# Performance work log

Hardware: AMD Instinct MI355X
Metric: run time of the kernel (lower is better)

## Reference

```python
import jax, jax.numpy as jnp
import numpy as np
from jax import lax

NPOINT = 1024
RADIUS = 0.2
NSAMPLE = 32
BN_EPS = 1e-3  # tf_util batch_norm variance_epsilon


def setup_inputs() -> dict:
    key = jax.random.key(0)
    ks = jax.random.split(key, 16)
    B, N, Cp = 8, 4096, 64
    mlp = [64, 64, 128]
    cin = 3 + Cp  # use_xyz=True concatenates local coords
    dk, dout = 128, 128
    inp = {}
    inp["xyz"] = jax.random.uniform(ks[0], (B, N, 3), jnp.float32)
    inp["points"] = jax.random.normal(ks[1], (B, N, Cp), jnp.float32)
    dims = [cin] + mlp
    for i in range(3):
        inp[f"W{i}"] = jax.random.normal(ks[2 + i], (dims[i], dims[i + 1]), jnp.float32) / np.sqrt(dims[i]).astype(np.float32)
        inp[f"b{i}"] = jnp.zeros((dims[i + 1],), jnp.float32)
        inp[f"g{i}"] = jnp.ones((dims[i + 1],), jnp.float32)
        inp[f"be{i}"] = jnp.zeros((dims[i + 1],), jnp.float32)
    inp["Wq"] = jax.random.normal(ks[10], (3, dk), jnp.float32) * 0.1
    inp["Wk"] = jax.random.normal(ks[11], (mlp[-1], dk), jnp.float32) * 0.1
    inp["Wv"] = jax.random.normal(ks[12], (mlp[-1], dout), jnp.float32) * 0.1
    return inp


def farthest_point_sample(xyz, npoint):
    # xyz: [B, N, 3] -> idx [B, npoint] (sequential FPS, seeded at point 0)
    B, N, _ = xyz.shape

    def body(carry, _):
        dist, farthest = carry  # dist [B,N], farthest [B]
        centroid = jnp.take_along_axis(xyz, farthest[:, None, None], axis=1)  # [B,1,3]
        d = jnp.sum((xyz - centroid) ** 2, axis=-1)  # [B,N]
        dist = jnp.minimum(dist, d)
        nxt = jnp.argmax(dist, axis=-1).astype(jnp.int32)
        return (dist, nxt), farthest

    init = (jnp.full((B, N), 1e10, xyz.dtype), jnp.zeros((B,), jnp.int32))
    _, idxs = lax.scan(body, init, None, length=npoint)
    return jnp.transpose(idxs)  # [B, npoint]


def query_ball_point(radius, nsample, xyz, new_xyz):
    # first `nsample` points (in index order) within radius; pad with first hit
    N = xyz.shape[1]
    d2 = jnp.sum((new_xyz[:, :, None, :] - xyz[:, None, :, :]) ** 2, axis=-1)  # [B,S,N]
    inball = d2 < radius * radius
    ar = jnp.arange(N, dtype=jnp.int32)
    order_key = jnp.where(inball, ar, ar + N)
    idx = jnp.argsort(order_key, axis=-1)[..., :nsample].astype(jnp.int32)  # [B,S,nsample]
    valid = jnp.take_along_axis(inball, idx, axis=-1)
    idx = jnp.where(valid, idx, idx[..., :1])
    return idx


def group_point(feat, idx):
    # feat [B,N,C], idx [B,S,K] -> [B,S,K,C]
    return jax.vmap(lambda f, i: f[i])(feat, idx)


def _conv_bn_relu(x, W, b, g, be):
    y = jnp.einsum('bskc,cd->bskd', x, W) + b  # 1x1 conv == pointwise linear
    mean = jnp.mean(y, axis=(0, 1, 2))
    var = jnp.var(y, axis=(0, 1, 2))
    y = (y - mean) * g * lax.rsqrt(var + BN_EPS) + be
    return jax.nn.relu(y)


def _forward(xyz, points, Ws, bs, gs, bes, Wq, Wk, Wv):
    fps_idx = farthest_point_sample(xyz, NPOINT)                 # [B,S]
    new_xyz = jnp.take_along_axis(xyz, fps_idx[..., None], 1)    # [B,S,3]
    idx = query_ball_point(RADIUS, NSAMPLE, xyz, new_xyz)        # [B,S,K]
    grouped_xyz = group_point(xyz, idx) - new_xyz[:, :, None, :]  # local coords
    grouped_pts = group_point(points, idx)
    new_points = jnp.concatenate([grouped_xyz, grouped_pts], axis=-1)  # [B,S,K,3+C]
    for W, b, g, be in zip(Ws, bs, gs, bes):
        new_points = _conv_bn_relu(new_points, W, b, g, be)
    # attention pooling over the K neighbors, query from group center coords
    dk = Wq.shape[1]
    q = new_xyz @ Wq                                         # [B,S,dk]
    k = jnp.einsum('bskc,cd->bskd', new_points, Wk)          # [B,S,K,dk]
    v = jnp.einsum('bskc,co->bsko', new_points, Wv)          # [B,S,K,out]
    scores = jax.nn.softmax(jnp.einsum('bsd,bskd->bsk', q, k) / jnp.sqrt(jnp.float32(dk)), axis=-1)
    pooled = jnp.einsum('bsk,bsko->bso', scores, v)          # [B,S,out]
    return new_xyz, pooled, idx


def reference(xyz, points, W0, b0, g0, be0, W1, b1, g1, be1, W2, b2, g2, be2, Wq, Wk, Wv):
    return _forward(xyz, points, (W0, W1, W2), (b0, b1, b2), (g0, g1, g2), (be0, be1, be2), Wq, Wk, Wv)
```

## Files before the change

kernel.cpp:

```cpp
#include <hip/hip_runtime.h>
#include <hip/hip_bf16.h>

#define DI __device__ __forceinline__

typedef __attribute__((ext_vector_type(8))) short bf16x8;
typedef __attribute__((ext_vector_type(4))) float f32x4;

DI float fmulr(float a, float b){ return __fmul_rn(a,b); }
DI float faddr(float a, float b){ return __fadd_rn(a,b); }
DI float fsubr(float a, float b){ return __fsub_rn(a,b); }
DI float dist2e(float x,float y,float z,float cx,float cy,float cz){
  float dx=fsubr(x,cx), dy=fsubr(y,cy), dz=fsubr(z,cz);
  return faddr(faddr(fmulr(dx,dx),fmulr(dy,dy)),fmulr(dz,dz));
}
DI unsigned short f2bf(float f){ __hip_bfloat16 h=__float2bfloat16(f); return *reinterpret_cast<unsigned short*>(&h); }
DI unsigned long long umax64(unsigned long long a, unsigned long long b){ return a>b?a:b; }

template<int C> DI float dmax_step(float x){
  int y=__builtin_amdgcn_update_dpp(0, __float_as_int(x), C, 0xF, 0xF, true);
  return fmaxf(x, __int_as_float(y));
}

__global__ __launch_bounds__(512) void fps_kernel(const float* __restrict__ xyz, float* __restrict__ out0){
  extern __shared__ char smem[];
  float4* sp4=(float4*)smem;
  float* spf=(float*)smem;
  unsigned long long* keys=(unsigned long long*)(smem+65536);
  int b=blockIdx.x, tid=threadIdx.x;
  const float* xb = xyz + (size_t)b*12288;
  for(int e=tid;e<12288;e+=512){ int p=e/3, c=e-3*p; spf[4*p+c]=xb[e]; }
  __syncthreads();
  float px[8],py[8],pz[8],dist[8];
  int p0=tid*8;
  #pragma unroll
  for(int j=0;j<8;j++){ float4 r=sp4[p0+j]; px[j]=r.x; py[j]=r.y; pz[j]=r.z; dist[j]=1e10f; }
  int cur=0;
  float4 cc0=sp4[0];
  float cx=cc0.x, cy=cc0.y, cz=cc0.z;
  int w=tid>>6, lane=tid&63;
  int c0s=0,c1s=0;
  float* ob = out0 + (size_t)b*1024*3;
  #pragma unroll 1
  for(int t=0;t<1024;t++){
    bool mine=((t&511)==tid);
    int hi=t>>9;
    c0s=(mine&&hi==0)?cur:c0s;
    c1s=(mine&&hi==1)?cur:c1s;
    float nd[8];
    #pragma unroll
    for(int j=0;j<8;j++){
      float d=dist2e(px[j],py[j],pz[j],cx,cy,cz);
      float m=fminf(dist[j],d); dist[j]=m; nd[j]=m;
    }
    float a0=fmaxf(nd[0],nd[1]), a1=fmaxf(nd[2],nd[3]), a2=fmaxf(nd[4],nd[5]), a3=fmaxf(nd[6],nd[7]);
    float bv=fmaxf(fmaxf(a0,a1),fmaxf(a2,a3));
    unsigned msk=0u;
    #pragma unroll
    for(int j=0;j<8;j++) msk |= (nd[j]==bv)?(1u<<j):0u;
    int bj=__ffs(msk)-1;
    int bi=p0+bj;
    float x=bv;
    x=dmax_step<0x111>(x); x=dmax_step<0x112>(x); x=dmax_step<0x114>(x); x=dmax_step<0x118>(x);
    x=dmax_step<0x142>(x); x=dmax_step<0x143>(x);
    float wv=__int_as_float(__builtin_amdgcn_readlane(__float_as_int(x),63));
    unsigned long long em=__ballot(bv==wv);
    int L=(int)(__ffsll(em)-1);
    int wbi=__builtin_amdgcn_readlane(bi,L);
    int par=t&1;
    if(lane==0){
      keys[par*8+w] = ((unsigned long long)__float_as_uint(wv)<<32)
                    | (unsigned long long)(0xFFFFFFFFu-(unsigned)wbi);
    }
    __syncthreads();
    const ulonglong2* sl2=(const ulonglong2*)(keys+par*8);
    ulonglong2 k0=sl2[0], k1=sl2[1], k2=sl2[2], k3=sl2[3];
    unsigned long long m0=umax64(k0.x,k0.y), m1=umax64(k1.x,k1.y);
    unsigned long long m2=umax64(k2.x,k2.y), m3=umax64(k3.x,k3.y);
    unsigned long long k =umax64(umax64(m0,m1),umax64(m2,m3));
    cur=(int)(0xFFFFFFFFu-(unsigned)(k&0xFFFFFFFFull));
    float4 cc=sp4[cur]; cx=cc.x; cy=cc.y; cz=cc.z;
  }
  { int t0=tid;     float4 c=sp4[c0s]; ob[t0*3]=c.x; ob[t0*3+1]=c.y; ob[t0*3+2]=c.z; }
  { int t1=tid+512; float4 c=sp4[c1s]; ob[t1*3]=c.x; ob[t1*3+1]=c.y; ob[t1*3+2]=c.z; }
}

__global__ __launch_bounds__(256) void ballq_kernel(const float* __restrict__ xyz, const float* __restrict__ out0,
        int* __restrict__ idxw, float* __restrict__ out2){
  __shared__ float sp[12288];
  int tid=threadIdx.x;
  int g = blockIdx.x*4 + (tid>>6);
  int lane = tid&63;
  int b = blockIdx.x>>8;
  const float* xb = xyz + (size_t)b*4096*3;
  const float4* src=(const float4*)xb; float4* dst=(float4*)sp;
  #pragma unroll
  for(int i=0;i<12;i++) dst[i*256+tid]=src[i*256+tid];
  __syncthreads();
  float cx=out0[(size_t)g*3], cy=out0[(size_t)g*3+1], cz=out0[(size_t)g*3+2];
  const float R2 = (float)(0.2*0.2);
  int cnt=0, firstp=0; bool haveFirst=false;
  for(int c=0;c<64;c++){
    int p=c*64+lane;
    float x=sp[3*p], y=sp[3*p+1], z=sp[3*p+2];
    float d2=dist2e(x,y,z,cx,cy,cz);
    bool inb = d2 < R2;
    unsigned long long mask=__ballot(inb);
    if(!haveFirst && mask){ firstp = c*64 + (__ffsll((unsigned long long)mask)-1); haveFirst=true; }
    int pos = cnt + (int)__popcll(mask & ((1ull<<lane)-1ull));
    if(inb && pos<32){ idxw[(size_t)g*32+pos]=p; out2[(size_t)g*32+pos]=(float)p; }
    cnt += (int)__popcll(mask);
    if(cnt>=32) break;
  }
  if(cnt<32){
    for(int j=cnt+lane; j<32; j+=64){ idxw[(size_t)g*32+j]=firstp; out2[(size_t)g*32+j]=(float)firstp; }
  }
}

__global__ void m_kernel(const float* __restrict__ Wq, const float* __restrict__ Wk, float* __restrict__ M){
  int c = threadIdx.x;
  float m0=0.f,m1=0.f,m2=0.f;
  for(int d=0; d<128; d++){
    float wk = Wk[c*128+d];
    m0 += Wq[d]*wk; m1 += Wq[128+d]*wk; m2 += Wq[256+d]*wk;
  }
  M[c]=m0; M[128+c]=m1; M[256+c]=m2;
}

__global__ __launch_bounds__(256) void l0_mfma(const float* __restrict__ xyz, const float* __restrict__ pts,
    const float* __restrict__ out0, const int* __restrict__ idxw,
    const float* __restrict__ W0, const float* __restrict__ b0,
    __hip_bfloat16* __restrict__ y0, float* __restrict__ P){
  __shared__ unsigned short xg[64*72];
  __shared__ unsigned short wt[64*72];
  __shared__ unsigned short yt[64*72];
  __shared__ float xyzl[64][4];
  __shared__ float w0c[3][64];
  __shared__ float ps[4][64];
  __shared__ float qs[4][64];
  int tid=threadIdx.x; int base=blockIdx.x*64;
  int w=tid>>6, lane=tid&63;
  for(int i=0;i<16;i++){
    int r=w*16+i; int R=base+r;
    int g=R>>5; int b=g>>10; int p=idxw[R];
    xg[r*72+lane] = f2bf(pts[((size_t)b*4096+(size_t)p)*64+lane]);
    if(lane<3) xyzl[r][lane] = fsubr(xyz[((size_t)b*4096+(size_t)p)*3+lane], out0[(size_t)g*3+lane]);
  }
  for(int e=tid; e<4096; e+=256){
    int k=e>>6, n=e&63;
    wt[n*72+k]=f2bf(W0[(3+k)*64+n]);
  }
  if(tid<192){ int r=tid>>6, n=tid&63; w0c[r][n]=W0[r*64+n]; }
  __syncthreads();
  int m=lane&15, kg=lane>>4;
  f32x4 acc[4];
  #pragma unroll
  for(int t=0;t<4;t++){
    int col=t*16+m;
    float bb=b0[col], wx=w0c[0][col], wy=w0c[1][col], wz=w0c[2][col];
    #pragma unroll
    for(int rg=0;rg<4;rg++){
      int row=w*16+kg*4+rg;
      acc[t][rg]=bb + xyzl[row][0]*wx + xyzl[row][1]*wy + xyzl[row][2]*wz;
    }
  }
  #pragma unroll
  for(int ks=0; ks<2; ks++){
    int k0=ks*32+kg*8;
    bf16x8 af = *(bf16x8*)&xg[(w*16+m)*72 + k0];
    #pragma unroll
    for(int t=0;t<4;t++){
      bf16x8 bfr = *(bf16x8*)&wt[(t*16+m)*72 + k0];
      acc[t]=__builtin_amdgcn_mfma_f32_16x16x32_bf16(af,bfr,acc[t],0,0,0);
    }
  }
  #pragma unroll
  for(int t=0;t<4;t++){
    float s=0.f,q=0.f;
    #pragma unroll
    for(int rg=0;rg<4;rg++){
      float v=acc[t][rg];
      s+=v; q+=v*v;
      yt[(w*16+kg*4+rg)*72 + t*16+m]=f2bf(v);
    }
    s+=__shfl_xor(s,16); q+=__shfl_xor(q,16);
    s+=__shfl_xor(s,32); q+=__shfl_xor(q,32);
    if(kg==0){ ps[w][t*16+m]=s; qs[w][t*16+m]=q; }
  }
  __syncthreads();
  if(tid<64){
    float s=ps[0][tid]+ps[1][tid]+ps[2][tid]+ps[3][tid];
    float q=qs[0][tid]+qs[1][tid]+qs[2][tid]+qs[3][tid];
    P[(size_t)tid*4096+blockIdx.x]=s;
    P[(size_t)(128+tid)*4096+blockIdx.x]=q;
  }
  for(int e=tid; e<512; e+=256){
    int r=e>>3, c0=(e&7)*8;
    *reinterpret_cast<uint4*>(y0 + ((size_t)base+r)*64 + c0) = *reinterpret_cast<uint4*>(&yt[r*72+c0]);
  }
}

template<int CIN,int COUT>
__global__ __launch_bounds__(256) void lmid_mfma(const __hip_bfloat16* __restrict__ xin,
    const float* __restrict__ ssIn, const float* __restrict__ W, const float* __restrict__ bias,
    __hip_bfloat16* __restrict__ yout, float* __restrict__ P){
  constexpr int XS = CIN+8;
  constexpr int YS = COUT+8;
  constexpr int NT = COUT/16;
  __shared__ unsigned short xt[64*XS];
  __shared__ unsigned short wt[COUT*XS];
  __shared__ unsigned short yt[64*YS];
  __shared__ float ps[4][COUT];
  __shared__ float qs[4][COUT];
  int tid=threadIdx.x; size_t base=(size_t)blockIdx.x*64;
  int w=tid>>6, lane=tid&63;
  for(int e=tid; e<64*CIN/8; e+=256){
    int r=e/(CIN/8), c0=(e%(CIN/8))*8;
    uint4 raw = *reinterpret_cast<const uint4*>(xin + (base+(size_t)r)*CIN + c0);
    unsigned u[4]={raw.x,raw.y,raw.z,raw.w};
    unsigned short* dst=&xt[r*XS+c0];
    #pragma unroll
    for(int k2=0;k2<4;k2++){
      int c=c0+2*k2;
      float lo=__uint_as_float(u[k2]<<16);
      float hi=__uint_as_float(u[k2]&0xFFFF0000u);
      float a=lo*ssIn[c]+ssIn[128+c]; a=a>0.f?a:0.f;
      float bq=hi*ssIn[c+1]+ssIn[128+c+1]; bq=bq>0.f?bq:0.f;
      dst[2*k2]=f2bf(a); dst[2*k2+1]=f2bf(bq);
    }
  }
  for(int e=tid; e<CIN*COUT; e+=256){
    int k=e/COUT, n=e-k*COUT;
    wt[n*XS+k]=f2bf(W[e]);
  }
  __syncthreads();
  f32x4 acc[NT];
  #pragma unroll
  for(int t=0;t<NT;t++) acc[t]=(f32x4){0.f,0.f,0.f,0.f};
  int m=lane&15, kg=lane>>4;
  #pragma unroll
  for(int ks=0; ks<CIN/32; ks++){
    int k0=ks*32+kg*8;
    bf16x8 af = *(bf16x8*)&xt[(w*16+m)*XS + k0];
    #pragma unroll
    for(int t=0;t<NT;t++){
      bf16x8 bfr = *(bf16x8*)&wt[(t*16+m)*XS + k0];
      acc[t]=__builtin_amdgcn_mfma_f32_16x16x32_bf16(af,bfr,acc[t],0,0,0);
    }
  }
  #pragma unroll
  for(int t=0;t<NT;t++){
    float bv=bias[t*16+m];
    float s=0.f,q=0.f;
    #pragma unroll
    for(int rg=0;rg<4;rg++){
      float v=acc[t][rg]+bv;
      s+=v; q+=v*v;
      yt[(w*16+kg*4+rg)*YS + t*16+m]=f2bf(v);
    }
    s+=__shfl_xor(s,16); q+=__shfl_xor(q,16);
    s+=__shfl_xor(s,32); q+=__shfl_xor(q,32);
    if(kg==0){ ps[w][t*16+m]=s; qs[w][t*16+m]=q; }
  }
  __syncthreads();
  if(tid<COUT){
    float s=ps[0][tid]+ps[1][tid]+ps[2][tid]+ps[3][tid];
    float q=qs[0][tid]+qs[1][tid]+qs[2][tid]+qs[3][tid];
    P[(size_t)tid*4096+blockIdx.x]=s;
    P[(size_t)(128+tid)*4096+blockIdx.x]=q;
  }
  for(int e=tid; e<64*COUT/8; e+=256){
    int r=e/(COUT/8), c0=(e%(COUT/8))*8;
    *reinterpret_cast<uint4*>(yout + (base+(size_t)r)*COUT + c0) = *reinterpret_cast<uint4*>(&yt[r*YS+c0]);
  }
}

__global__ void fin_kernel(const float* __restrict__ P, const float* __restrict__ gg, const float* __restrict__ be,
                           float* __restrict__ ss){
  int ch=blockIdx.x; int lane=threadIdx.x;
  float s=0.f,q=0.f;
  for(int blk=lane; blk<4096; blk+=64){ s+=P[(size_t)ch*4096+blk]; q+=P[(size_t)(128+ch)*4096+blk]; }
  #pragma unroll
  for(int m=32;m>=1;m>>=1){ s+=__shfl_xor(s,m); q+=__shfl_xor(q,m); }
  if(lane==0){
    const float invNT = 1.0f/262144.0f;
    float mean=s*invNT; float var=q*invNT - mean*mean;
    float scale=gg[ch]/sqrtf(var+1e-3f);
    ss[ch]=scale; ss[128+ch]=be[ch]-mean*scale;
  }
}

__global__ __launch_bounds__(256) void sh_kernel(const __hip_bfloat16* __restrict__ y2,
    const float* __restrict__ ss2, const float* __restrict__ M, const float* __restrict__ out0,
    float* __restrict__ hbar){
  __shared__ float h[2][32*130];
  __shared__ float uLds[2][128];
  __shared__ float sLds[2][32];
  __shared__ float partLds[2][4][32];
  int tid=threadIdx.x; int grp=tid>>7, t=tid&127;
  size_t g=(size_t)blockIdx.x*2+grp;
  #pragma unroll
  for(int i=0;i<4;i++){
    int e=i*128+t;
    int row=e>>4, c0=(e&15)*8;
    uint4 raw=*reinterpret_cast<const uint4*>(y2+(g*32+(size_t)row)*128+c0);
    unsigned u[4]={raw.x,raw.y,raw.z,raw.w};
    #pragma unroll
    for(int k=0;k<4;k++){
      int c=c0+2*k;
      float lo=__uint_as_float(u[k]<<16), hi=__uint_as_float(u[k]&0xFFFF0000u);
      float a=lo*ss2[c]+ss2[128+c]; float bq=hi*ss2[c+1]+ss2[128+c+1];
      h[grp][row*130+c]  = a>0.f?a:0.f;
      h[grp][row*130+c+1]= bq>0.f?bq:0.f;
    }
  }
  float cx=out0[g*3], cy=out0[g*3+1], cz=out0[g*3+2];
  uLds[grp][t]=cx*M[t]+cy*M[128+t]+cz*M[256+t];
  __syncthreads();
  {
    int row=t&31, q=t>>5;
    float sc=0.f;
    const float* hr=&h[grp][row*130];
    const float* ur=&uLds[grp][0];
    #pragma unroll
    for(int c=0;c<32;c++) sc += hr[q*32+c]*ur[q*32+c];
    partLds[grp][q][row]=sc;
  }
  __syncthreads();
  if(t<32){
    float s=(partLds[grp][0][t]+partLds[grp][1][t])+(partLds[grp][2][t]+partLds[grp][3][t]);
    s*=0.08838834764831845f;
    float mx=s;
    #pragma unroll
    for(int m=16;m>=1;m>>=1) mx=fmaxf(mx,__shfl_xor(mx,m));
    float p=expf(s-mx);
    float sum=p;
    #pragma unroll
    for(int m=16;m>=1;m>>=1) sum+=__shfl_xor(sum,m);
    sLds[grp][t]=p/sum;
  }
  __syncthreads();
  float hb=0.f;
  for(int k=0;k<32;k++) hb+=sLds[grp][k]*h[grp][k*130+t];
  hbar[g*128+t]=hb;
}

__global__ __launch_bounds__(256) void pool_kernel(const float* __restrict__ hbar, const float* __restrict__ Wv,
    float* __restrict__ out1){
  __shared__ float xl[32*129];
  int tid=threadIdx.x; size_t g0=(size_t)blockIdx.x*32;
  for(int e=tid;e<32*128;e+=256){ int r=e>>7,ch=e&127; xl[r*129+ch]=hbar[(g0+(size_t)r)*128+ch]; }
  __syncthreads();
  int r=tid&31;
  int cgu=__builtin_amdgcn_readfirstlane(tid>>5);
  float acc[16];
  #pragma unroll
  for(int j=0;j<16;j++) acc[j]=0.f;
  for(int c=0;c<128;c++){
    float xv=xl[r*129+c];
    #pragma unroll
    for(int j=0;j<16;j++) acc[j]+=xv*Wv[c*128+cgu*16+j];
  }
  #pragma unroll
  for(int j=0;j<16;j++) out1[(g0+(size_t)r)*128+cgu*16+j]=acc[j];
}

extern "C" void kernel_launch(void* const* d_in, const int* in_sizes, int n_in,
                              void* d_out, int out_size, void* d_ws, size_t ws_size,
                              hipStream_t stream){
  (void)in_sizes; (void)n_in; (void)out_size; (void)ws_size;
  const float* xyz=(const float*)d_in[0];
  const float* pts=(const float*)d_in[1];
  const float* W0=(const float*)d_in[2];  const float* b0=(const float*)d_in[3];
  const float* g0=(const float*)d_in[4];  const float* be0=(const float*)d_in[5];
  const float* W1=(const float*)d_in[6];  const float* b1=(const float*)d_in[7];
  const float* g1=(const float*)d_in[8];  const float* be1=(const float*)d_in[9];
  const float* W2=(const float*)d_in[10]; const float* b2=(const float*)d_in[11];
  const float* g2=(const float*)d_in[12]; const float* be2=(const float*)d_in[13];
  const float* Wq=(const float*)d_in[14]; const float* Wk=(const float*)d_in[15];
  const float* Wv=(const float*)d_in[16];
  float* out0=(float*)d_out;
  float* out1=out0 + (size_t)8*1024*3;
  float* out2=out1 + (size_t)8192*128;

  char* ws=(char*)d_ws; size_t off=0;
  int* idxw=(int*)(ws+off);                    off += (size_t)8192*32*4;
  __hip_bfloat16* fa=(__hip_bfloat16*)(ws+off); off += (size_t)262144*64*2;
  __hip_bfloat16* fb=(__hip_bfloat16*)(ws+off); off += (size_t)262144*64*2;
  __hip_bfloat16* fc=(__hip_bfloat16*)(ws+off); off += (size_t)262144*128*2;
  float* P =(float*)(ws+off);                  off += (size_t)256*4096*4;
  float* ss0=(float*)(ws+off);                 off += 256*4;
  float* ss1=(float*)(ws+off);                 off += 256*4;
  float* ss2=(float*)(ws+off);                 off += 256*4;
  float* M =(float*)(ws+off);                  off += 3*128*4 + 128;
  float* hb=(float*)(ws+off);                  off += (size_t)8192*128*4;

  hipLaunchKernelGGL(fps_kernel,   dim3(8),    dim3(512), 65536+128, stream, xyz, out0);
  hipLaunchKernelGGL(ballq_kernel, dim3(2048), dim3(256),  0, stream, xyz, out0, idxw, out2);
  hipLaunchKernelGGL(m_kernel,     dim3(1),    dim3(128),  0, stream, Wq, Wk, M);
  hipLaunchKernelGGL(l0_mfma,      dim3(4096), dim3(256),  0, stream, xyz, pts, out0, idxw, W0, b0, fa, P);
  hipLaunchKernelGGL(fin_kernel,   dim3(64),   dim3(64),   0, stream, P, g0, be0, ss0);
  hipLaunchKernelGGL((lmid_mfma<64,64>),  dim3(4096), dim3(256), 0, stream, fa, ss0, W1, b1, fb, P);
  hipLaunchKernelGGL(fin_kernel,   dim3(64),   dim3(64),   0, stream, P, g1, be1, ss1);
  hipLaunchKernelGGL((lmid_mfma<64,128>), dim3(4096), dim3(256), 0, stream, fb, ss1, W2, b2, fc, P);
  hipLaunchKernelGGL(fin_kernel,   dim3(128),  dim3(64),   0, stream, P, g2, be2, ss2);
  hipLaunchKernelGGL(sh_kernel,    dim3(4096), dim3(256),  0, stream, fc, ss2, M, out0, hb);
  hipLaunchKernelGGL(pool_kernel,  dim3(256),  dim3(256),  0, stream, hb, Wv, out1);
}
```

Baseline: 891.0 us.

## Halve FPS block to four waves and broadcast winner coords; cache BN scales in LDS

```diff
diff --git a/kernel.cpp b/kernel.cpp
--- a/kernel.cpp
+++ b/kernel.cpp
@@ -14,49 +14,53 @@
   return faddr(faddr(fmulr(dx,dx),fmulr(dy,dy)),fmulr(dz,dz));
 }
 DI unsigned short f2bf(float f){ __hip_bfloat16 h=__float2bfloat16(f); return *reinterpret_cast<unsigned short*>(&h); }
-DI unsigned long long umax64(unsigned long long a, unsigned long long b){ return a>b?a:b; }
 
 template<int C> DI float dmax_step(float x){
   int y=__builtin_amdgcn_update_dpp(0, __float_as_int(x), C, 0xF, 0xF, true);
   return fmaxf(x, __int_as_float(y));
 }
 
-__global__ __launch_bounds__(512) void fps_kernel(const float* __restrict__ xyz, float* __restrict__ out0){
+__global__ __launch_bounds__(256) void fps_kernel(const float* __restrict__ xyz, float* __restrict__ out0){
   extern __shared__ char smem[];
   float4* sp4=(float4*)smem;
   float* spf=(float*)smem;
   unsigned long long* keys=(unsigned long long*)(smem+65536);
+  float4* wco=(float4*)(smem+65536+64);
   int b=blockIdx.x, tid=threadIdx.x;
   const float* xb = xyz + (size_t)b*12288;
-  for(int e=tid;e<12288;e+=512){ int p=e/3, c=e-3*p; spf[4*p+c]=xb[e]; }
-  __syncthreads();
-  float px[8],py[8],pz[8],dist[8];
-  int p0=tid*8;
-  #pragma unroll
-  for(int j=0;j<8;j++){ float4 r=sp4[p0+j]; px[j]=r.x; py[j]=r.y; pz[j]=r.z; dist[j]=1e10f; }
+  for(int e=tid;e<12288;e+=256){ int p=e/3, c=e-3*p; spf[4*p+c]=xb[e]; }
+  __syncthreads();
+  float px[16],py[16],pz[16],dist[16];
+  int p0 = tid*16;
+  #pragma unroll
+  for(int j=0;j<16;j++){ float4 r=sp4[p0+j]; px[j]=r.x; py[j]=r.y; pz[j]=r.z; dist[j]=1e10f; }
   int cur=0;
   float4 cc0=sp4[0];
   float cx=cc0.x, cy=cc0.y, cz=cc0.z;
   int w=tid>>6, lane=tid&63;
-  int c0s=0,c1s=0;
+  int c0s=0,c1s=0,c2s=0,c3s=0;
   float* ob = out0 + (size_t)b*1024*3;
   #pragma unroll 1
   for(int t=0;t<1024;t++){
-    bool mine=((t&511)==tid);
-    int hi=t>>9;
-    c0s=(mine&&hi==0)?cur:c0s;
-    c1s=(mine&&hi==1)?cur:c1s;
-    float nd[8];
-    #pragma unroll
-    for(int j=0;j<8;j++){
+    bool mine = ((t&255)==tid);
+    int hi = t>>8;
+    c0s = (mine && hi==0) ? cur : c0s;
+    c1s = (mine && hi==1) ? cur : c1s;
+    c2s = (mine && hi==2) ? cur : c2s;
+    c3s = (mine && hi==3) ? cur : c3s;
+    float nd[16];
+    #pragma unroll
+    for(int j=0;j<16;j++){
       float d=dist2e(px[j],py[j],pz[j],cx,cy,cz);
       float m=fminf(dist[j],d); dist[j]=m; nd[j]=m;
     }
     float a0=fmaxf(nd[0],nd[1]), a1=fmaxf(nd[2],nd[3]), a2=fmaxf(nd[4],nd[5]), a3=fmaxf(nd[6],nd[7]);
-    float bv=fmaxf(fmaxf(a0,a1),fmaxf(a2,a3));
+    float a4=fmaxf(nd[8],nd[9]), a5=fmaxf(nd[10],nd[11]), a6=fmaxf(nd[12],nd[13]), a7=fmaxf(nd[14],nd[15]);
+    float b0=fmaxf(a0,a1), b1=fmaxf(a2,a3), b2=fmaxf(a4,a5), b3=fmaxf(a6,a7);
+    float bv=fmaxf(fmaxf(b0,b1),fmaxf(b2,b3));
     unsigned msk=0u;
     #pragma unroll
-    for(int j=0;j<8;j++) msk |= (nd[j]==bv)?(1u<<j):0u;
+    for(int j=0;j<16;j++) msk |= (nd[j]==bv) ? (1u<<j) : 0u;
     int bj=__ffs(msk)-1;
     int bi=p0+bj;
     float x=bv;
@@ -65,23 +69,29 @@
     float wv=__int_as_float(__builtin_amdgcn_readlane(__float_as_int(x),63));
     unsigned long long em=__ballot(bv==wv);
     int L=(int)(__ffsll(em)-1);
-    int wbi=__builtin_amdgcn_readlane(bi,L);
     int par=t&1;
-    if(lane==0){
-      keys[par*8+w] = ((unsigned long long)__float_as_uint(wv)<<32)
-                    | (unsigned long long)(0xFFFFFFFFu-(unsigned)wbi);
+    if(lane==L){
+      keys[par*4+w] = ((unsigned long long)__float_as_uint(wv)<<32)
+                    | (unsigned long long)(0xFFFFFFFFu-(unsigned)bi);
+      wco[par*4+w]  = make_float4(px[bj],py[bj],pz[bj],0.f);
     }
     __syncthreads();
-    const ulonglong2* sl2=(const ulonglong2*)(keys+par*8);
-    ulonglong2 k0=sl2[0], k1=sl2[1], k2=sl2[2], k3=sl2[3];
-    unsigned long long m0=umax64(k0.x,k0.y), m1=umax64(k1.x,k1.y);
-    unsigned long long m2=umax64(k2.x,k2.y), m3=umax64(k3.x,k3.y);
-    unsigned long long k =umax64(umax64(m0,m1),umax64(m2,m3));
+    ulonglong2 ka=*(const ulonglong2*)(keys+par*4);
+    ulonglong2 kb=*(const ulonglong2*)(keys+par*4+2);
+    float4 q0=wco[par*4+0], q1=wco[par*4+1], q2=wco[par*4+2], q3=wco[par*4+3];
+    bool s01 = ka.x>=ka.y; unsigned long long k01 = s01?ka.x:ka.y;
+    bool s23 = kb.x>=kb.y; unsigned long long k23 = s23?kb.x:kb.y;
+    float c01x=s01?q0.x:q1.x, c01y=s01?q0.y:q1.y, c01z=s01?q0.z:q1.z;
+    float c23x=s23?q2.x:q3.x, c23y=s23?q2.y:q3.y, c23z=s23?q2.z:q3.z;
+    bool sf = k01>=k23;
+    unsigned long long k = sf?k01:k23;
+    cx = sf?c01x:c23x; cy = sf?c01y:c23y; cz = sf?c01z:c23z;
     cur=(int)(0xFFFFFFFFu-(unsigned)(k&0xFFFFFFFFull));
-    float4 cc=sp4[cur]; cx=cc.x; cy=cc.y; cz=cc.z;
   }
   { int t0=tid;     float4 c=sp4[c0s]; ob[t0*3]=c.x; ob[t0*3+1]=c.y; ob[t0*3+2]=c.z; }
-  { int t1=tid+512; float4 c=sp4[c1s]; ob[t1*3]=c.x; ob[t1*3+1]=c.y; ob[t1*3+2]=c.z; }
+  { int t1=tid+256; float4 c=sp4[c1s]; ob[t1*3]=c.x; ob[t1*3+1]=c.y; ob[t1*3+2]=c.z; }
+  { int t2=tid+512; float4 c=sp4[c2s]; ob[t2*3]=c.x; ob[t2*3+1]=c.y; ob[t2*3+2]=c.z; }
+  { int t3=tid+768; float4 c=sp4[c3s]; ob[t3*3]=c.x; ob[t3*3+1]=c.y; ob[t3*3+2]=c.z; }
 }
 
 __global__ __launch_bounds__(256) void ballq_kernel(const float* __restrict__ xyz, const float* __restrict__ out0,
@@ -211,8 +221,11 @@
   __shared__ unsigned short yt[64*YS];
   __shared__ float ps[4][COUT];
   __shared__ float qs[4][COUT];
+  __shared__ float ssl[256];
   int tid=threadIdx.x; size_t base=(size_t)blockIdx.x*64;
   int w=tid>>6, lane=tid&63;
+  ssl[tid]=ssIn[tid];
+  __syncthreads();
   for(int e=tid; e<64*CIN/8; e+=256){
     int r=e/(CIN/8), c0=(e%(CIN/8))*8;
     uint4 raw = *reinterpret_cast<const uint4*>(xin + (base+(size_t)r)*CIN + c0);
@@ -223,8 +236,8 @@
       int c=c0+2*k2;
       float lo=__uint_as_float(u[k2]<<16);
       float hi=__uint_as_float(u[k2]&0xFFFF0000u);
-      float a=lo*ssIn[c]+ssIn[128+c]; a=a>0.f?a:0.f;
-      float bq=hi*ssIn[c+1]+ssIn[128+c+1]; bq=bq>0.f?bq:0.f;
+      float a=lo*ssl[c]+ssl[128+c]; a=a>0.f?a:0.f;
+      float bq=hi*ssl[c+1]+ssl[128+c+1]; bq=bq>0.f?bq:0.f;
       dst[2*k2]=f2bf(a); dst[2*k2+1]=f2bf(bq);
     }
   }
@@ -296,8 +309,11 @@
   __shared__ float uLds[2][128];
   __shared__ float sLds[2][32];
   __shared__ float partLds[2][4][32];
+  __shared__ float ssl[256];
   int tid=threadIdx.x; int grp=tid>>7, t=tid&127;
   size_t g=(size_t)blockIdx.x*2+grp;
+  ssl[tid]=ss2[tid];
+  __syncthreads();
   #pragma unroll
   for(int i=0;i<4;i++){
     int e=i*128+t;
@@ -308,7 +324,7 @@
     for(int k=0;k<4;k++){
       int c=c0+2*k;
       float lo=__uint_as_float(u[k]<<16), hi=__uint_as_float(u[k]&0xFFFF0000u);
-      float a=lo*ss2[c]+ss2[128+c]; float bq=hi*ss2[c+1]+ss2[128+c+1];
+      float a=lo*ssl[c]+ssl[128+c]; float bq=hi*ssl[c+1]+ssl[128+c+1];
       h[grp][row*130+c]  = a>0.f?a:0.f;
       h[grp][row*130+c+1]= bq>0.f?bq:0.f;
     }
@@ -394,7 +410,7 @@
   float* M =(float*)(ws+off);                  off += 3*128*4 + 128;
   float* hb=(float*)(ws+off);                  off += (size_t)8192*128*4;
 
-  hipLaunchKernelGGL(fps_kernel,   dim3(8),    dim3(512), 65536+128, stream, xyz, out0);
+  hipLaunchKernelGGL(fps_kernel,   dim3(8),    dim3(256), 65536+64+128, stream, xyz, out0);
   hipLaunchKernelGGL(ballq_kernel, dim3(2048), dim3(256),  0, stream, xyz, out0, idxw, out2);
   hipLaunchKernelGGL(m_kernel,     dim3(1),    dim3(128),  0, stream, Wq, Wk, M);
   hipLaunchKernelGGL(l0_mfma,      dim3(4096), dim3(256),  0, stream, xyz, pts, out0, idxw, W0, b0, fa, P);
```

New measurement: 1.504 ms. +68.7%, slower.
